# Kernel optimization log

Hardware: AMD Instinct MI355X
Metric: run time of the kernel (lower is better)

The kernel has to match this reference:

```python
import jax, jax.numpy as jnp
import numpy as np

B, H, N, D, RPE = 2, 8, 4096, 64, 64
LAYERS = 3


def _rms(x):
    # SimpleRMSNorm: x / sqrt(mean(x^2) + eps), no learned scale
    return x / jnp.sqrt(jnp.mean(x * x, axis=-1, keepdims=True) + 1e-8)


def setup_inputs() -> dict:
    key = jax.random.key(0)
    ks = jax.random.split(key, 7)
    s = 1.0 / np.sqrt(RPE)
    return {
        "x": jax.random.normal(ks[0], (B, H, N, D), dtype=jnp.float32),
        "w_in": jax.random.normal(ks[1], (1, RPE), dtype=jnp.float32) * 0.5,
        "b_in": jax.random.normal(ks[2], (RPE,), dtype=jnp.float32) * 0.02,
        "w_hid": jax.random.normal(ks[3], (LAYERS, RPE, RPE), dtype=jnp.float32) * s,
        "b_hid": jax.random.normal(ks[4], (LAYERS, RPE), dtype=jnp.float32) * 0.02,
        "w_out": jax.random.normal(ks[5], (RPE, H * D), dtype=jnp.float32) * s,
        "b_out": jax.random.normal(ks[6], (H * D,), dtype=jnp.float32) * 0.02,
    }


def reference(x, w_in, b_in, w_hid, b_hid, w_out, b_out):
    n = x.shape[-2]
    dt = x.dtype

    def rpe(idx):  # idx: (m, 1) relative-position features
        h = idx @ w_in + b_in  # (m, RPE)
        for i in range(LAYERS):  # non-residual: x = layer(x)
            h = jax.nn.relu(_rms(h)) @ w_hid[i] + b_hid[i]
        h = jax.nn.relu(_rms(h)) @ w_out + b_out  # (m, H*D)
        return h.reshape(-1, H, D).transpose(1, 0, 2)  # (H, m, D)

    zero_idx = jnp.ones((1, 1), dt)
    pos_idx = (1.0 / jnp.arange(2, n + 1, dtype=dt)).reshape(n - 1, 1)
    neg_idx = (-1.0 / jnp.arange(n, 1, -1, dtype=dt)).reshape(n - 1, 1)

    zero_k = rpe(zero_idx)  # (H, 1, D); used for both T[0] slots like the torch code
    a = jnp.concatenate([zero_k, rpe(pos_idx), zero_k, rpe(neg_idx)], axis=1)  # (H, 2n, D)
    # act_type='none' -> identity activation on a

    # Toeplitz matvec as circular conv of length 2n via FFT
    y = jnp.fft.rfft(x, 2 * n, axis=-2)          # (B, H, n+1, D) complex
    v = jnp.fft.rfft(a, 2 * n, axis=-2)[None]    # (1, H, n+1, D) complex
    out = jnp.fft.irfft(v * y, 2 * n, axis=-2)[:, :, :n, :]
    return out.astype(dt)
```

## Files before the change

### kernel.cpp

```cpp
#include <hip/hip_runtime.h>

#define N_SEQ 4096
#define N_FFT 8192
#define LAYERS 3
#define FT 512
#define PIDX(i) ((i) + ((i) >> 5))

template<int M>
__device__ inline void pass16_fwd(float* re, float* im, int tid)
{
    const int Q = M >> 4;
    const int j = tid & (Q - 1);
    const int G = tid / Q;
    const int base = G * M + j;
    float xr[4][4], xi[4][4];
#pragma unroll
    for (int a = 0; a < 4; ++a)
#pragma unroll
        for (int b = 0; b < 4; ++b) {
            int idx = PIDX(base + a * (M >> 2) + b * Q);
            xr[a][b] = re[idx]; xi[a][b] = im[idx];
        }
    const float w1 = -6.283185307179586f / (float)M;
#pragma unroll
    for (int b = 0; b < 4; ++b) {
        float ar = xr[0][b] + xr[2][b], ai = xi[0][b] + xi[2][b];
        float br = xr[0][b] - xr[2][b], bi = xi[0][b] - xi[2][b];
        float cr = xr[1][b] + xr[3][b], ci = xi[1][b] + xi[3][b];
        float dr = xi[1][b] - xi[3][b], di = -(xr[1][b] - xr[3][b]);
        float c1, s1; __sincosf(w1 * (float)(b * Q + j), &s1, &c1);
        float c2 = c1 * c1 - s1 * s1, s2 = 2.f * c1 * s1;
        float c3 = c2 * c1 - s2 * s1, s3 = c2 * s1 + s2 * c1;
        xr[0][b] = ar + cr;               xi[0][b] = ai + ci;
        float t1r = br + dr, t1i = bi + di;
        xr[1][b] = t1r * c1 - t1i * s1;   xi[1][b] = t1r * s1 + t1i * c1;
        float t2r = ar - cr, t2i = ai - ci;
        xr[2][b] = t2r * c2 - t2i * s2;   xi[2][b] = t2r * s2 + t2i * c2;
        float t3r = br - dr, t3i = bi - di;
        xr[3][b] = t3r * c3 - t3i * s3;   xi[3][b] = t3r * s3 + t3i * c3;
    }
    {
        const float w4 = -6.283185307179586f / (float)(M >> 2);
        float c1, s1; __sincosf(w4 * (float)j, &s1, &c1);
        float c2 = c1 * c1 - s1 * s1, s2 = 2.f * c1 * s1;
        float c3 = c2 * c1 - s2 * s1, s3 = c2 * s1 + s2 * c1;
#pragma unroll
        for (int a = 0; a < 4; ++a) {
            float ar = xr[a][0] + xr[a][2], ai = xi[a][0] + xi[a][2];
            float br = xr[a][0] - xr[a][2], bi = xi[a][0] - xi[a][2];
            float cr = xr[a][1] + xr[a][3], ci = xi[a][1] + xi[a][3];
            float dr = xi[a][1] - xi[a][3], di = -(xr[a][1] - xr[a][3]);
            xr[a][0] = ar + cr;               xi[a][0] = ai + ci;
            float t1r = br + dr, t1i = bi + di;
            xr[a][1] = t1r * c1 - t1i * s1;   xi[a][1] = t1r * s1 + t1i * c1;
            float t2r = ar - cr, t2i = ai - ci;
            xr[a][2] = t2r * c2 - t2i * s2;   xi[a][2] = t2r * s2 + t2i * c2;
            float t3r = br - dr, t3i = bi - di;
            xr[a][3] = t3r * c3 - t3i * s3;   xi[a][3] = t3r * s3 + t3i * c3;
        }
    }
#pragma unroll
    for (int a = 0; a < 4; ++a)
#pragma unroll
        for (int b = 0; b < 4; ++b) {
            int idx = PIDX(base + a * (M >> 2) + b * Q);
            re[idx] = xr[a][b]; im[idx] = xi[a][b];
        }
}

template<int M>
__device__ inline void pass16_inv(float* re, float* im, int tid)
{
    const int Q = M >> 4;
    const int j = tid & (Q - 1);
    const int G = tid / Q;
    const int base = G * M + j;
    float xr[4][4], xi[4][4];
#pragma unroll
    for (int a = 0; a < 4; ++a)
#pragma unroll
        for (int b = 0; b < 4; ++b) {
            int idx = PIDX(base + a * (M >> 2) + b * Q);
            xr[a][b] = re[idx]; xi[a][b] = im[idx];
        }
    {
        const float w4 = 6.283185307179586f / (float)(M >> 2);
        float c1, s1; __sincosf(w4 * (float)j, &s1, &c1);
        float c2 = c1 * c1 - s1 * s1, s2 = 2.f * c1 * s1;
        float c3 = c2 * c1 - s2 * s1, s3 = c2 * s1 + s2 * c1;
#pragma unroll
        for (int a = 0; a < 4; ++a) {
            float t0r = xr[a][0], t0i = xi[a][0];
            float t1r = xr[a][1] * c1 - xi[a][1] * s1, t1i = xr[a][1] * s1 + xi[a][1] * c1;
            float t2r = xr[a][2] * c2 - xi[a][2] * s2, t2i = xr[a][2] * s2 + xi[a][2] * c2;
            float t3r = xr[a][3] * c3 - xi[a][3] * s3, t3i = xr[a][3] * s3 + xi[a][3] * c3;
            float pr = t0r + t2r, pi = t0i + t2i;
            float qr = t0r - t2r, qi = t0i - t2i;
            float rr = t1r + t3r, ri = t1i + t3i;
            float sr = -(t1i - t3i), si = t1r - t3r;
            xr[a][0] = pr + rr; xi[a][0] = pi + ri;
            xr[a][1] = qr + sr; xi[a][1] = qi + si;
            xr[a][2] = pr - rr; xi[a][2] = pi - ri;
            xr[a][3] = qr - sr; xi[a][3] = qi - si;
        }
    }
    const float w1 = 6.283185307179586f / (float)M;
#pragma unroll
    for (int b = 0; b < 4; ++b) {
        float c1, s1; __sincosf(w1 * (float)(b * Q + j), &s1, &c1);
        float c2 = c1 * c1 - s1 * s1, s2 = 2.f * c1 * s1;
        float c3 = c2 * c1 - s2 * s1, s3 = c2 * s1 + s2 * c1;
        float t0r = xr[0][b], t0i = xi[0][b];
        float t1r = xr[1][b] * c1 - xi[1][b] * s1, t1i = xr[1][b] * s1 + xi[1][b] * c1;
        float t2r = xr[2][b] * c2 - xi[2][b] * s2, t2i = xr[2][b] * s2 + xi[2][b] * c2;
        float t3r = xr[3][b] * c3 - xi[3][b] * s3, t3i = xr[3][b] * s3 + xi[3][b] * c3;
        float pr = t0r + t2r, pi = t0i + t2i;
        float qr = t0r - t2r, qi = t0i - t2i;
        float rr = t1r + t3r, ri = t1i + t3i;
        float sr = -(t1i - t3i), si = t1r - t3r;
        xr[0][b] = pr + rr; xi[0][b] = pi + ri;
        xr[1][b] = qr + sr; xi[1][b] = qi + si;
        xr[2][b] = pr - rr; xi[2][b] = pi - ri;
        xr[3][b] = qr - sr; xi[3][b] = qi - si;
    }
#pragma unroll
    for (int a = 0; a < 4; ++a)
#pragma unroll
        for (int b = 0; b < 4; ++b) {
            int idx = PIDX(base + a * (M >> 2) + b * Q);
            re[idx] = xr[a][b]; im[idx] = xi[a][b];
        }
}

__device__ inline void fwd8(float* zr, float* zi, int o)
{
    const float R = 0.70710678118654752f;
    {
        float ar = zr[o] + zr[o+4], ai = zi[o] + zi[o+4];
        float br = zr[o] - zr[o+4], bi = zi[o] - zi[o+4];
        float cr = zr[o+2] + zr[o+6], ci = zi[o+2] + zi[o+6];
        float dr = zi[o+2] - zi[o+6], di = -(zr[o+2] - zr[o+6]);
        zr[o]   = ar + cr; zi[o]   = ai + ci;
        zr[o+2] = br + dr; zi[o+2] = bi + di;
        zr[o+4] = ar - cr; zi[o+4] = ai - ci;
        zr[o+6] = br - dr; zi[o+6] = bi - di;
    }
    {
        float ar = zr[o+1] + zr[o+5], ai = zi[o+1] + zi[o+5];
        float br = zr[o+1] - zr[o+5], bi = zi[o+1] - zi[o+5];
        float cr = zr[o+3] + zr[o+7], ci = zi[o+3] + zi[o+7];
        float dr = zi[o+3] - zi[o+7], di = -(zr[o+3] - zr[o+7]);
        zr[o+1] = ar + cr; zi[o+1] = ai + ci;
        float t1r = br + dr, t1i = bi + di;
        zr[o+3] = R * (t1r + t1i); zi[o+3] = R * (t1i - t1r);
        float t2r = ar - cr, t2i = ai - ci;
        zr[o+5] = t2i;  zi[o+5] = -t2r;
        float t3r = br - dr, t3i = bi - di;
        zr[o+7] = R * (t3i - t3r); zi[o+7] = -R * (t3r + t3i);
    }
#pragma unroll
    for (int p = 0; p < 8; p += 2) {
        float ur = zr[o+p], ui = zi[o+p], vr = zr[o+p+1], vi = zi[o+p+1];
        zr[o+p]   = ur + vr; zi[o+p]   = ui + vi;
        zr[o+p+1] = ur - vr; zi[o+p+1] = ui - vi;
    }
}

__device__ inline void inv8(float* zr, float* zi, int o)
{
    const float R = 0.70710678118654752f;
#pragma unroll
    for (int p = 0; p < 8; p += 2) {
        float ur = zr[o+p], ui = zi[o+p], vr = zr[o+p+1], vi = zi[o+p+1];
        zr[o+p]   = ur + vr; zi[o+p]   = ui + vi;
        zr[o+p+1] = ur - vr; zi[o+p+1] = ui - vi;
    }
    {
        float t0r = zr[o],   t0i = zi[o];
        float t1r = zr[o+2], t1i = zi[o+2];
        float t2r = zr[o+4], t2i = zi[o+4];
        float t3r = zr[o+6], t3i = zi[o+6];
        float pr = t0r + t2r, pi = t0i + t2i;
        float qr = t0r - t2r, qi = t0i - t2i;
        float rr = t1r + t3r, ri = t1i + t3i;
        float sr = -(t1i - t3i), si = t1r - t3r;
        zr[o]   = pr + rr; zi[o]   = pi + ri;
        zr[o+2] = qr + sr; zi[o+2] = qi + si;
        zr[o+4] = pr - rr; zi[o+4] = pi - ri;
        zr[o+6] = qr - sr; zi[o+6] = qi - si;
    }
    {
        float t0r = zr[o+1], t0i = zi[o+1];
        float yr = zr[o+3], yi = zi[o+3];
        float t1r = R * (yr - yi), t1i = R * (yr + yi);
        yr = zr[o+5]; yi = zi[o+5];
        float t2r = -yi, t2i = yr;
        yr = zr[o+7]; yi = zi[o+7];
        float t3r = -R * (yr + yi), t3i = R * (yr - yi);
        float pr = t0r + t2r, pi = t0i + t2i;
        float qr = t0r - t2r, qi = t0i - t2i;
        float rr = t1r + t3r, ri = t1i + t3i;
        float sr = -(t1i - t3i), si = t1r - t3r;
        zr[o+1] = pr + rr; zi[o+1] = pi + ri;
        zr[o+3] = qr + sr; zi[o+3] = qi + si;
        zr[o+5] = pr - rr; zi[o+5] = pi - ri;
        zr[o+7] = qr - sr; zi[o+7] = qi - si;
    }
}

__global__ __launch_bounds__(256) void rpe_hidden_kernel(
    const float* __restrict__ w_in, const float* __restrict__ b_in,
    const float* __restrict__ w_hid, const float* __restrict__ b_hid,
    float* __restrict__ u_t)
{
    __shared__ float4 wl[1024];
    __shared__ float ubuf[64][65];
    __shared__ float sums[64][5];
    const int tid = threadIdx.x;
    const int p   = tid & 63;
    const int qr  = tid >> 6;
    const int pos = blockIdx.x * 64 + p;

    float v;
    if (pos == 0 || pos == N_SEQ) v = 1.0f;
    else if (pos < N_SEQ)         v = 1.0f / (float)(pos + 1);
    else                          v = -1.0f / (float)(2 * N_SEQ + 1 - pos);

    float h[16];
#pragma unroll
    for (int i = 0; i < 16; ++i) {
        int f = qr * 16 + i;
        h[i] = v * w_in[f] + b_in[f];
    }
    for (int L = 0; L < LAYERS; ++L) {
        const float4* wsrc = (const float4*)(w_hid + L * 4096);
#pragma unroll
        for (int i = 0; i < 4; ++i) wl[i * 256 + tid] = wsrc[i * 256 + tid];
        float s = 0.f;
#pragma unroll
        for (int i = 0; i < 16; ++i) s += h[i] * h[i];
        sums[p][qr] = s;
        __syncthreads();
        float tot = sums[p][0] + sums[p][1] + sums[p][2] + sums[p][3];
        float r = rsqrtf(tot * (1.f / 64.f) + 1e-8f);
#pragma unroll
        for (int i = 0; i < 16; ++i)
            ubuf[p][qr * 16 + i] = fmaxf(h[i] * r, 0.f);
        __syncthreads();
        float acc[16];
#pragma unroll
        for (int i = 0; i < 16; ++i) acc[i] = b_hid[L * 64 + qr * 16 + i];
#pragma unroll 4
        for (int j = 0; j < 64; ++j) {
            float uj = ubuf[p][j];
            float4 w0 = wl[j * 16 + qr * 4 + 0];
            float4 w1 = wl[j * 16 + qr * 4 + 1];
            float4 w2 = wl[j * 16 + qr * 4 + 2];
            float4 w3 = wl[j * 16 + qr * 4 + 3];
            acc[0]  = fmaf(uj, w0.x, acc[0]);  acc[1]  = fmaf(uj, w0.y, acc[1]);
            acc[2]  = fmaf(uj, w0.z, acc[2]);  acc[3]  = fmaf(uj, w0.w, acc[3]);
            acc[4]  = fmaf(uj, w1.x, acc[4]);  acc[5]  = fmaf(uj, w1.y, acc[5]);
            acc[6]  = fmaf(uj, w1.z, acc[6]);  acc[7]  = fmaf(uj, w1.w, acc[7]);
            acc[8]  = fmaf(uj, w2.x, acc[8]);  acc[9]  = fmaf(uj, w2.y, acc[9]);
            acc[10] = fmaf(uj, w2.z, acc[10]); acc[11] = fmaf(uj, w2.w, acc[11]);
            acc[12] = fmaf(uj, w3.x, acc[12]); acc[13] = fmaf(uj, w3.y, acc[13]);
            acc[14] = fmaf(uj, w3.z, acc[14]); acc[15] = fmaf(uj, w3.w, acc[15]);
        }
#pragma unroll
        for (int i = 0; i < 16; ++i) h[i] = acc[i];
        __syncthreads();
    }
    float s = 0.f;
#pragma unroll
    for (int i = 0; i < 16; ++i) s += h[i] * h[i];
    sums[p][qr] = s;
    __syncthreads();
    float tot = sums[p][0] + sums[p][1] + sums[p][2] + sums[p][3];
    float r = rsqrtf(tot * (1.f / 64.f) + 1e-8f);
#pragma unroll
    for (int i = 0; i < 16; ++i)
        u_t[(size_t)(qr * 16 + i) * N_FFT + pos] = fmaxf(h[i] * r, 0.f);
}

__global__ __launch_bounds__(256) void rpe_out_kernel(
    const float* __restrict__ u_t, const float* __restrict__ w_out,
    const float* __restrict__ b_out, float* __restrict__ a_t)
{
    __shared__ float4 wl[1024];
    const int tid = threadIdx.x;
    const int c   = blockIdx.y;
    const int pos = blockIdx.x * 256 + tid;
    for (int i = tid; i < 1024; i += 256) {
        int j = i >> 4, q = i & 15;
        wl[i] = *(const float4*)(w_out + j * 512 + c * 64 + q * 4);
    }
    float acc[64];
#pragma unroll
    for (int f = 0; f < 64; ++f) acc[f] = b_out[c * 64 + f];
    __syncthreads();
#pragma unroll 2
    for (int j = 0; j < 64; ++j) {
        float uj = u_t[(size_t)j * N_FFT + pos];
#pragma unroll
        for (int q = 0; q < 16; ++q) {
            float4 w4 = wl[j * 16 + q];
            acc[q * 4 + 0] = fmaf(uj, w4.x, acc[q * 4 + 0]);
            acc[q * 4 + 1] = fmaf(uj, w4.y, acc[q * 4 + 1]);
            acc[q * 4 + 2] = fmaf(uj, w4.z, acc[q * 4 + 2]);
            acc[q * 4 + 3] = fmaf(uj, w4.w, acc[q * 4 + 3]);
        }
    }
#pragma unroll
    for (int f = 0; f < 64; ++f)
        a_t[(size_t)(c * 64 + f) * N_FFT + pos] = acc[f];
}

__global__ __launch_bounds__(FT, 4) void fft_a_kernel(const float* __restrict__ a_t,
                                                      float2* __restrict__ Af)
{
    __shared__ float re[8448];
    __shared__ float im[8448];
    const int tid = threadIdx.x;
    const size_t row = blockIdx.x;
    const float* src = a_t + row * N_FFT;
    const float wstep = -6.283185307179586f / 8192.f;
#pragma unroll
    for (int k = tid; k < 2048; k += FT) {
        float x0 = src[k], x1 = src[k + 2048], x2 = src[k + 4096], x3 = src[k + 6144];
        float ar = x0 + x2, br = x0 - x2;
        float cr = x1 + x3, e = x1 - x3;
        re[PIDX(k)] = ar + cr; im[PIDX(k)] = 0.f;
        float c1, s1; __sincosf(wstep * (float)k, &s1, &c1);
        float c2 = c1 * c1 - s1 * s1, s2 = 2.f * c1 * s1;
        float c3 = c2 * c1 - s2 * s1, s3 = c2 * s1 + s2 * c1;
        re[PIDX(k + 2048)] = br * c1 + e * s1;  im[PIDX(k + 2048)] = br * s1 - e * c1;
        float t2r = ar - cr;
        re[PIDX(k + 4096)] = t2r * c2;          im[PIDX(k + 4096)] = t2r * s2;
        re[PIDX(k + 6144)] = br * c3 - e * s3;  im[PIDX(k + 6144)] = br * s3 + e * c3;
    }
    __syncthreads();
    pass16_fwd<2048>(re, im, tid);
    __syncthreads();
    pass16_fwd<128>(re, im, tid);
    __syncthreads();
    float zr[16], zi[16];
    const int base = tid * 16;
#pragma unroll
    for (int c = 0; c < 16; ++c) { int idx = PIDX(base + c); zr[c] = re[idx]; zi[c] = im[idx]; }
    fwd8(zr, zi, 0); fwd8(zr, zi, 8);
    const float inv = 1.0f / (float)N_FFT;
    float4* dst4 = (float4*)(Af + row * N_FFT + base);
#pragma unroll
    for (int q = 0; q < 8; ++q)
        dst4[q] = make_float4(zr[2*q] * inv, zi[2*q] * inv, zr[2*q+1] * inv, zi[2*q+1] * inv);
}

__global__ __launch_bounds__(256) void transpose_x_kernel(const float* __restrict__ x,
                                                          float2* __restrict__ xt2)
{
    __shared__ float t0[64][65];
    __shared__ float t1[64][65];
    int h = blockIdx.x >> 6;
    int nb = blockIdx.x & 63;
    int lx = threadIdx.x & 63;
    int ly = threadIdx.x >> 6;
    const float* s0 = x + ((size_t)h * N_SEQ + nb * 64) * 64;
    const float* s1 = x + ((size_t)(8 + h) * N_SEQ + nb * 64) * 64;
    for (int r = ly; r < 64; r += 4) {
        t0[r][lx] = s0[r * 64 + lx];
        t1[r][lx] = s1[r * 64 + lx];
    }
    __syncthreads();
    for (int r = ly; r < 64; r += 4) {
        float2* dst = xt2 + (size_t)(h * 64 + r) * N_SEQ + nb * 64;
        dst[lx] = make_float2(t0[lx][r], t1[lx][r]);
    }
}

__global__ __launch_bounds__(FT, 4) void conv_kernel(const float2* __restrict__ xt2,
                                                     const float2* __restrict__ Af,
                                                     float2* __restrict__ out_t2)
{
    __shared__ float re[8448];
    __shared__ float im[8448];
    const int tid = threadIdx.x;
    const int hd = blockIdx.x;
    const float2* src = xt2 + (size_t)hd * N_SEQ;
    {
        const float wstep = -6.283185307179586f / 8192.f;
#pragma unroll
        for (int k = tid; k < 2048; k += FT) {
            float2 z0 = src[k], z1 = src[k + 2048];
            float ar = z0.x, ai = z0.y;
            float cr = z1.x, ci = z1.y;
            float dr = z1.y, di = -z1.x;
            re[PIDX(k)] = ar + cr; im[PIDX(k)] = ai + ci;
            float c1, s1; __sincosf(wstep * (float)k, &s1, &c1);
            float c2 = c1 * c1 - s1 * s1, s2 = 2.f * c1 * s1;
            float c3 = c2 * c1 - s2 * s1, s3 = c2 * s1 + s2 * c1;
            float t1r = ar + dr, t1i = ai + di;
            re[PIDX(k + 2048)] = t1r * c1 - t1i * s1; im[PIDX(k + 2048)] = t1r * s1 + t1i * c1;
            float t2r = ar - cr, t2i = ai - ci;
            re[PIDX(k + 4096)] = t2r * c2 - t2i * s2; im[PIDX(k + 4096)] = t2r * s2 + t2i * c2;
            float t3r = ar - dr, t3i = ai - di;
            re[PIDX(k + 6144)] = t3r * c3 - t3i * s3; im[PIDX(k + 6144)] = t3r * s3 + t3i * c3;
        }
    }
    __syncthreads();
    pass16_fwd<2048>(re, im, tid);
    __syncthreads();
    pass16_fwd<128>(re, im, tid);
    __syncthreads();
    {
        float zr[16], zi[16];
        const int base = tid * 16;
#pragma unroll
        for (int c = 0; c < 16; ++c) { int idx = PIDX(base + c); zr[c] = re[idx]; zi[c] = im[idx]; }
        fwd8(zr, zi, 0); fwd8(zr, zi, 8);
        const float4* af4 = (const float4*)(Af + (size_t)hd * N_FFT + base);
#pragma unroll
        for (int q = 0; q < 8; ++q) {
            float4 a4 = af4[q];
            float xr = zr[2*q], xi_ = zi[2*q];
            zr[2*q]   = xr * a4.x - xi_ * a4.y;  zi[2*q]   = xr * a4.y + xi_ * a4.x;
            xr = zr[2*q+1]; xi_ = zi[2*q+1];
            zr[2*q+1] = xr * a4.z - xi_ * a4.w;  zi[2*q+1] = xr * a4.w + xi_ * a4.z;
        }
        inv8(zr, zi, 0); inv8(zr, zi, 8);
#pragma unroll
        for (int c = 0; c < 16; ++c) { int idx = PIDX(base + c); re[idx] = zr[c]; im[idx] = zi[c]; }
    }
    __syncthreads();
    pass16_inv<128>(re, im, tid);
    __syncthreads();
    pass16_inv<2048>(re, im, tid);
    __syncthreads();
    {
        const float wstep = 6.283185307179586f / 8192.f;
        float2* dst = out_t2 + (size_t)hd * N_SEQ;
#pragma unroll
        for (int k = tid; k < 2048; k += FT) {
            float c1, s1; __sincosf(wstep * (float)k, &s1, &c1);
            float c2 = c1 * c1 - s1 * s1, s2 = 2.f * c1 * s1;
            float c3 = c2 * c1 - s2 * s1, s3 = c2 * s1 + s2 * c1;
            float t0r = re[PIDX(k)],        t0i = im[PIDX(k)];
            float y1r = re[PIDX(k + 2048)], y1i = im[PIDX(k + 2048)];
            float y2r = re[PIDX(k + 4096)], y2i = im[PIDX(k + 4096)];
            float y3r = re[PIDX(k + 6144)], y3i = im[PIDX(k + 6144)];
            float t1r = y1r * c1 - y1i * s1, t1i = y1r * s1 + y1i * c1;
            float t2r = y2r * c2 - y2i * s2, t2i = y2r * s2 + y2i * c2;
            float t3r = y3r * c3 - y3i * s3, t3i = y3r * s3 + y3i * c3;
            float pr = t0r + t2r, pi = t0i + t2i;
            float qr = t0r - t2r, qi = t0i - t2i;
            float rr = t1r + t3r, ri = t1i + t3i;
            float sr = -(t1i - t3i), si = t1r - t3r;
            dst[k]        = make_float2(pr + rr, pi + ri);
            dst[k + 2048] = make_float2(qr + sr, qi + si);
        }
    }
}

__global__ __launch_bounds__(256) void transpose_o_kernel(const float2* __restrict__ out_t2,
                                                          float* __restrict__ out)
{
    __shared__ float t0[64][65];
    __shared__ float t1[64][65];
    int h = blockIdx.x >> 6;
    int nb = blockIdx.x & 63;
    int lx = threadIdx.x & 63;
    int ly = threadIdx.x >> 6;
    for (int r = ly; r < 64; r += 4) {
        float2 v = out_t2[(size_t)(h * 64 + r) * N_SEQ + nb * 64 + lx];
        t0[r][lx] = v.x;
        t1[r][lx] = v.y;
    }
    __syncthreads();
    float* d0 = out + ((size_t)h * N_SEQ + nb * 64) * 64;
    float* d1 = out + ((size_t)(8 + h) * N_SEQ + nb * 64) * 64;
    for (int r = ly; r < 64; r += 4) {
        d0[r * 64 + lx] = t0[lx][r];
        d1[r * 64 + lx] = t1[lx][r];
    }
}

extern "C" void kernel_launch(void* const* d_in, const int* in_sizes, int n_in,
                              void* d_out, int out_size, void* d_ws, size_t ws_size,
                              hipStream_t stream)
{
    const float* x     = (const float*)d_in[0];
    const float* w_in  = (const float*)d_in[1];
    const float* b_in  = (const float*)d_in[2];
    const float* w_hid = (const float*)d_in[3];
    const float* b_hid = (const float*)d_in[4];
    const float* w_out = (const float*)d_in[5];
    const float* b_out = (const float*)d_in[6];
    float* out = (float*)d_out;

    char* ws = (char*)d_ws;
    float2* Af    = (float2*)ws;
    float2* xt2   = (float2*)(ws + (size_t)32 * 1024 * 1024);
    float*  a_t   = (float*)(ws + (size_t)48 * 1024 * 1024);
    float*  u_t   = (float*)xt2;
    float2* out_t2 = (float2*)a_t;

    rpe_hidden_kernel<<<128, 256, 0, stream>>>(w_in, b_in, w_hid, b_hid, u_t);
    rpe_out_kernel<<<dim3(32, 8), 256, 0, stream>>>(u_t, w_out, b_out, a_t);
    fft_a_kernel<<<512, FT, 0, stream>>>(a_t, Af);
    transpose_x_kernel<<<512, 256, 0, stream>>>(x, xt2);
    conv_kernel<<<512, FT, 0, stream>>>(xt2, Af, out_t2);
    transpose_o_kernel<<<512, 256, 0, stream>>>(out_t2, out);
}
```

Baseline: 174.3 us.

## Fuse RPE MLP, x transpose, and kernel FFT into fewer launches

Merges the RPE hidden layers and output projection into one prep kernel that also runs the x transpose on extra blocks. The kernel FFT moves into the conv kernel, where the filter spectrum is kept in registers instead of being written to and read back from global memory. Per-element __sincosf calls in the FFT passes are replaced by one sincos per thread plus constant rotations and recurrences. This cuts launches and global traffic, but raises register pressure in conv_kernel, repeats the filter FFT inside every conv block, and may slightly reduce twiddle accuracy.

```diff
diff --git a/kernel.cpp b/kernel.cpp
--- a/kernel.cpp
+++ b/kernel.cpp
@@ -13,6 +13,8 @@
     const int j = tid & (Q - 1);
     const int G = tid / Q;
     const int base = G * M + j;
+    const float KR[4] = {1.f, 0.9238795325f, 0.7071067812f, 0.3826834324f};
+    const float KI[4] = {0.f, -0.3826834324f, -0.7071067812f, -0.9238795325f};
     float xr[4][4], xi[4][4];
 #pragma unroll
     for (int a = 0; a < 4; ++a)
@@ -21,16 +23,18 @@
             int idx = PIDX(base + a * (M >> 2) + b * Q);
             xr[a][b] = re[idx]; xi[a][b] = im[idx];
         }
-    const float w1 = -6.283185307179586f / (float)M;
+    float cj, sj;
+    __sincosf(-6.283185307179586f / (float)M * (float)j, &sj, &cj);
 #pragma unroll
     for (int b = 0; b < 4; ++b) {
+        float c1 = cj * KR[b] - sj * KI[b];
+        float s1 = cj * KI[b] + sj * KR[b];
+        float c2 = c1 * c1 - s1 * s1, s2 = 2.f * c1 * s1;
+        float c3 = c2 * c1 - s2 * s1, s3 = c2 * s1 + s2 * c1;
         float ar = xr[0][b] + xr[2][b], ai = xi[0][b] + xi[2][b];
         float br = xr[0][b] - xr[2][b], bi = xi[0][b] - xi[2][b];
         float cr = xr[1][b] + xr[3][b], ci = xi[1][b] + xi[3][b];
         float dr = xi[1][b] - xi[3][b], di = -(xr[1][b] - xr[3][b]);
-        float c1, s1; __sincosf(w1 * (float)(b * Q + j), &s1, &c1);
-        float c2 = c1 * c1 - s1 * s1, s2 = 2.f * c1 * s1;
-        float c3 = c2 * c1 - s2 * s1, s3 = c2 * s1 + s2 * c1;
         xr[0][b] = ar + cr;               xi[0][b] = ai + ci;
         float t1r = br + dr, t1i = bi + di;
         xr[1][b] = t1r * c1 - t1i * s1;   xi[1][b] = t1r * s1 + t1i * c1;
@@ -40,8 +44,8 @@
         xr[3][b] = t3r * c3 - t3i * s3;   xi[3][b] = t3r * s3 + t3i * c3;
     }
     {
-        const float w4 = -6.283185307179586f / (float)(M >> 2);
-        float c1, s1; __sincosf(w4 * (float)j, &s1, &c1);
+        float e1c = cj * cj - sj * sj, e1s = 2.f * cj * sj;
+        float c1 = e1c * e1c - e1s * e1s, s1 = 2.f * e1c * e1s;
         float c2 = c1 * c1 - s1 * s1, s2 = 2.f * c1 * s1;
         float c3 = c2 * c1 - s2 * s1, s3 = c2 * s1 + s2 * c1;
 #pragma unroll
@@ -75,6 +79,8 @@
     const int j = tid & (Q - 1);
     const int G = tid / Q;
     const int base = G * M + j;
+    const float KR[4] = {1.f, 0.9238795325f, 0.7071067812f, 0.3826834324f};
+    const float KI[4] = {0.f, 0.3826834324f, 0.7071067812f, 0.9238795325f};
     float xr[4][4], xi[4][4];
 #pragma unroll
     for (int a = 0; a < 4; ++a)
@@ -83,9 +89,11 @@
             int idx = PIDX(base + a * (M >> 2) + b * Q);
             xr[a][b] = re[idx]; xi[a][b] = im[idx];
         }
-    {
-        const float w4 = 6.283185307179586f / (float)(M >> 2);
-        float c1, s1; __sincosf(w4 * (float)j, &s1, &c1);
+    float cj, sj;
+    __sincosf(6.283185307179586f / (float)M * (float)j, &sj, &cj);
+    {
+        float e1c = cj * cj - sj * sj, e1s = 2.f * cj * sj;
+        float c1 = e1c * e1c - e1s * e1s, s1 = 2.f * e1c * e1s;
         float c2 = c1 * c1 - s1 * s1, s2 = 2.f * c1 * s1;
         float c3 = c2 * c1 - s2 * s1, s3 = c2 * s1 + s2 * c1;
 #pragma unroll
@@ -104,10 +112,10 @@
             xr[a][3] = qr - sr; xi[a][3] = qi - si;
         }
     }
-    const float w1 = 6.283185307179586f / (float)M;
 #pragma unroll
     for (int b = 0; b < 4; ++b) {
-        float c1, s1; __sincosf(w1 * (float)(b * Q + j), &s1, &c1);
+        float c1 = cj * KR[b] - sj * KI[b];
+        float s1 = cj * KI[b] + sj * KR[b];
         float c2 = c1 * c1 - s1 * s1, s2 = 2.f * c1 * s1;
         float c3 = c2 * c1 - s2 * s1, s3 = c2 * s1 + s2 * c1;
         float t0r = xr[0][b], t0i = xi[0][b];
@@ -208,28 +216,54 @@
     }
 }
 
-__global__ __launch_bounds__(256) void rpe_hidden_kernel(
+__global__ __launch_bounds__(256) void prep_kernel(
+    const float* __restrict__ x,
     const float* __restrict__ w_in, const float* __restrict__ b_in,
     const float* __restrict__ w_hid, const float* __restrict__ b_hid,
-    float* __restrict__ u_t)
-{
-    __shared__ float4 wl[1024];
-    __shared__ float ubuf[64][65];
-    __shared__ float sums[64][5];
+    const float* __restrict__ w_out, const float* __restrict__ b_out,
+    float* __restrict__ a_t, float2* __restrict__ xt2)
+{
+    __shared__ __align__(16) char smem[33536];
     const int tid = threadIdx.x;
-    const int p   = tid & 63;
-    const int qr  = tid >> 6;
-    const int pos = blockIdx.x * 64 + p;
+
+    if (blockIdx.x >= 256) {
+        float (*t0)[65] = (float (*)[65])smem;
+        float (*t1)[65] = (float (*)[65])(smem + 16640);
+        int bb = blockIdx.x - 256;
+        int h = bb >> 6;
+        int nb = bb & 63;
+        int lx = tid & 63;
+        int ly = tid >> 6;
+        const float* s0 = x + ((size_t)h * N_SEQ + nb * 64) * 64;
+        const float* s1 = x + ((size_t)(8 + h) * N_SEQ + nb * 64) * 64;
+        for (int r = ly; r < 64; r += 4) {
+            t0[r][lx] = s0[r * 64 + lx];
+            t1[r][lx] = s1[r * 64 + lx];
+        }
+        __syncthreads();
+        for (int r = ly; r < 64; r += 4) {
+            float2* dst = xt2 + (size_t)(h * 64 + r) * N_SEQ + nb * 64;
+            dst[lx] = make_float2(t0[lx][r], t1[lx][r]);
+        }
+        return;
+    }
+
+    float4* wl       = (float4*)smem;
+    float (*ubuf)[65] = (float (*)[65])(smem + 16384);
+    float (*sums)[9]  = (float (*)[9])(smem + 24704);
+    const int p   = tid & 31;
+    const int oct = tid >> 5;
+    const int pos = blockIdx.x * 32 + p;
 
     float v;
     if (pos == 0 || pos == N_SEQ) v = 1.0f;
     else if (pos < N_SEQ)         v = 1.0f / (float)(pos + 1);
     else                          v = -1.0f / (float)(2 * N_SEQ + 1 - pos);
 
-    float h[16];
-#pragma unroll
-    for (int i = 0; i < 16; ++i) {
-        int f = qr * 16 + i;
+    float h[8];
+#pragma unroll
+    for (int i = 0; i < 8; ++i) {
+        int f = oct * 8 + i;
         h[i] = v * w_in[f] + b_in[f];
     }
     for (int L = 0; L < LAYERS; ++L) {
@@ -238,164 +272,142 @@
         for (int i = 0; i < 4; ++i) wl[i * 256 + tid] = wsrc[i * 256 + tid];
         float s = 0.f;
 #pragma unroll
-        for (int i = 0; i < 16; ++i) s += h[i] * h[i];
-        sums[p][qr] = s;
-        __syncthreads();
-        float tot = sums[p][0] + sums[p][1] + sums[p][2] + sums[p][3];
+        for (int i = 0; i < 8; ++i) s += h[i] * h[i];
+        sums[p][oct] = s;
+        __syncthreads();
+        float tot = 0.f;
+#pragma unroll
+        for (int g = 0; g < 8; ++g) tot += sums[p][g];
         float r = rsqrtf(tot * (1.f / 64.f) + 1e-8f);
 #pragma unroll
-        for (int i = 0; i < 16; ++i)
-            ubuf[p][qr * 16 + i] = fmaxf(h[i] * r, 0.f);
-        __syncthreads();
-        float acc[16];
-#pragma unroll
-        for (int i = 0; i < 16; ++i) acc[i] = b_hid[L * 64 + qr * 16 + i];
+        for (int i = 0; i < 8; ++i)
+            ubuf[p][oct * 8 + i] = fmaxf(h[i] * r, 0.f);
+        __syncthreads();
+        float acc[8];
+#pragma unroll
+        for (int i = 0; i < 8; ++i) acc[i] = b_hid[L * 64 + oct * 8 + i];
 #pragma unroll 4
         for (int j = 0; j < 64; ++j) {
             float uj = ubuf[p][j];
-            float4 w0 = wl[j * 16 + qr * 4 + 0];
-            float4 w1 = wl[j * 16 + qr * 4 + 1];
-            float4 w2 = wl[j * 16 + qr * 4 + 2];
-            float4 w3 = wl[j * 16 + qr * 4 + 3];
-            acc[0]  = fmaf(uj, w0.x, acc[0]);  acc[1]  = fmaf(uj, w0.y, acc[1]);
-            acc[2]  = fmaf(uj, w0.z, acc[2]);  acc[3]  = fmaf(uj, w0.w, acc[3]);
-            acc[4]  = fmaf(uj, w1.x, acc[4]);  acc[5]  = fmaf(uj, w1.y, acc[5]);
-            acc[6]  = fmaf(uj, w1.z, acc[6]);  acc[7]  = fmaf(uj, w1.w, acc[7]);
-            acc[8]  = fmaf(uj, w2.x, acc[8]);  acc[9]  = fmaf(uj, w2.y, acc[9]);
-            acc[10] = fmaf(uj, w2.z, acc[10]); acc[11] = fmaf(uj, w2.w, acc[11]);
-            acc[12] = fmaf(uj, w3.x, acc[12]); acc[13] = fmaf(uj, w3.y, acc[13]);
-            acc[14] = fmaf(uj, w3.z, acc[14]); acc[15] = fmaf(uj, w3.w, acc[15]);
-        }
-#pragma unroll
-        for (int i = 0; i < 16; ++i) h[i] = acc[i];
-        __syncthreads();
-    }
-    float s = 0.f;
-#pragma unroll
-    for (int i = 0; i < 16; ++i) s += h[i] * h[i];
-    sums[p][qr] = s;
-    __syncthreads();
-    float tot = sums[p][0] + sums[p][1] + sums[p][2] + sums[p][3];
-    float r = rsqrtf(tot * (1.f / 64.f) + 1e-8f);
-#pragma unroll
-    for (int i = 0; i < 16; ++i)
-        u_t[(size_t)(qr * 16 + i) * N_FFT + pos] = fmaxf(h[i] * r, 0.f);
-}
-
-__global__ __launch_bounds__(256) void rpe_out_kernel(
-    const float* __restrict__ u_t, const float* __restrict__ w_out,
-    const float* __restrict__ b_out, float* __restrict__ a_t)
-{
-    __shared__ float4 wl[1024];
-    const int tid = threadIdx.x;
-    const int c   = blockIdx.y;
-    const int pos = blockIdx.x * 256 + tid;
-    for (int i = tid; i < 1024; i += 256) {
-        int j = i >> 4, q = i & 15;
-        wl[i] = *(const float4*)(w_out + j * 512 + c * 64 + q * 4);
-    }
-    float acc[64];
-#pragma unroll
-    for (int f = 0; f < 64; ++f) acc[f] = b_out[c * 64 + f];
-    __syncthreads();
-#pragma unroll 2
-    for (int j = 0; j < 64; ++j) {
-        float uj = u_t[(size_t)j * N_FFT + pos];
-#pragma unroll
-        for (int q = 0; q < 16; ++q) {
-            float4 w4 = wl[j * 16 + q];
-            acc[q * 4 + 0] = fmaf(uj, w4.x, acc[q * 4 + 0]);
-            acc[q * 4 + 1] = fmaf(uj, w4.y, acc[q * 4 + 1]);
-            acc[q * 4 + 2] = fmaf(uj, w4.z, acc[q * 4 + 2]);
-            acc[q * 4 + 3] = fmaf(uj, w4.w, acc[q * 4 + 3]);
-        }
-    }
-#pragma unroll
-    for (int f = 0; f < 64; ++f)
-        a_t[(size_t)(c * 64 + f) * N_FFT + pos] = acc[f];
-}
-
-__global__ __launch_bounds__(FT, 4) void fft_a_kernel(const float* __restrict__ a_t,
-                                                      float2* __restrict__ Af)
-{
-    __shared__ float re[8448];
-    __shared__ float im[8448];
-    const int tid = threadIdx.x;
-    const size_t row = blockIdx.x;
-    const float* src = a_t + row * N_FFT;
-    const float wstep = -6.283185307179586f / 8192.f;
-#pragma unroll
-    for (int k = tid; k < 2048; k += FT) {
-        float x0 = src[k], x1 = src[k + 2048], x2 = src[k + 4096], x3 = src[k + 6144];
-        float ar = x0 + x2, br = x0 - x2;
-        float cr = x1 + x3, e = x1 - x3;
-        re[PIDX(k)] = ar + cr; im[PIDX(k)] = 0.f;
-        float c1, s1; __sincosf(wstep * (float)k, &s1, &c1);
-        float c2 = c1 * c1 - s1 * s1, s2 = 2.f * c1 * s1;
-        float c3 = c2 * c1 - s2 * s1, s3 = c2 * s1 + s2 * c1;
-        re[PIDX(k + 2048)] = br * c1 + e * s1;  im[PIDX(k + 2048)] = br * s1 - e * c1;
-        float t2r = ar - cr;
-        re[PIDX(k + 4096)] = t2r * c2;          im[PIDX(k + 4096)] = t2r * s2;
-        re[PIDX(k + 6144)] = br * c3 - e * s3;  im[PIDX(k + 6144)] = br * s3 + e * c3;
-    }
-    __syncthreads();
-    pass16_fwd<2048>(re, im, tid);
-    __syncthreads();
-    pass16_fwd<128>(re, im, tid);
-    __syncthreads();
-    float zr[16], zi[16];
-    const int base = tid * 16;
-#pragma unroll
-    for (int c = 0; c < 16; ++c) { int idx = PIDX(base + c); zr[c] = re[idx]; zi[c] = im[idx]; }
-    fwd8(zr, zi, 0); fwd8(zr, zi, 8);
-    const float inv = 1.0f / (float)N_FFT;
-    float4* dst4 = (float4*)(Af + row * N_FFT + base);
-#pragma unroll
-    for (int q = 0; q < 8; ++q)
-        dst4[q] = make_float4(zr[2*q] * inv, zi[2*q] * inv, zr[2*q+1] * inv, zi[2*q+1] * inv);
-}
-
-__global__ __launch_bounds__(256) void transpose_x_kernel(const float* __restrict__ x,
-                                                          float2* __restrict__ xt2)
-{
-    __shared__ float t0[64][65];
-    __shared__ float t1[64][65];
-    int h = blockIdx.x >> 6;
-    int nb = blockIdx.x & 63;
-    int lx = threadIdx.x & 63;
-    int ly = threadIdx.x >> 6;
-    const float* s0 = x + ((size_t)h * N_SEQ + nb * 64) * 64;
-    const float* s1 = x + ((size_t)(8 + h) * N_SEQ + nb * 64) * 64;
-    for (int r = ly; r < 64; r += 4) {
-        t0[r][lx] = s0[r * 64 + lx];
-        t1[r][lx] = s1[r * 64 + lx];
-    }
-    __syncthreads();
-    for (int r = ly; r < 64; r += 4) {
-        float2* dst = xt2 + (size_t)(h * 64 + r) * N_SEQ + nb * 64;
-        dst[lx] = make_float2(t0[lx][r], t1[lx][r]);
-    }
-}
-
-__global__ __launch_bounds__(FT, 4) void conv_kernel(const float2* __restrict__ xt2,
-                                                     const float2* __restrict__ Af,
+            float4 w0 = wl[j * 16 + oct * 2];
+            float4 w1 = wl[j * 16 + oct * 2 + 1];
+            acc[0] = fmaf(uj, w0.x, acc[0]); acc[1] = fmaf(uj, w0.y, acc[1]);
+            acc[2] = fmaf(uj, w0.z, acc[2]); acc[3] = fmaf(uj, w0.w, acc[3]);
+            acc[4] = fmaf(uj, w1.x, acc[4]); acc[5] = fmaf(uj, w1.y, acc[5]);
+            acc[6] = fmaf(uj, w1.z, acc[6]); acc[7] = fmaf(uj, w1.w, acc[7]);
+        }
+#pragma unroll
+        for (int i = 0; i < 8; ++i) h[i] = acc[i];
+        __syncthreads();
+    }
+    {
+        float s = 0.f;
+#pragma unroll
+        for (int i = 0; i < 8; ++i) s += h[i] * h[i];
+        sums[p][oct] = s;
+        __syncthreads();
+        float tot = 0.f;
+#pragma unroll
+        for (int g = 0; g < 8; ++g) tot += sums[p][g];
+        float r = rsqrtf(tot * (1.f / 64.f) + 1e-8f);
+#pragma unroll
+        for (int i = 0; i < 8; ++i)
+            ubuf[p][oct * 8 + i] = fmaxf(h[i] * r, 0.f);
+        __syncthreads();
+    }
+    for (int c = 0; c < 8; ++c) {
+        float4 wreg[4];
+#pragma unroll
+        for (int cc = 0; cc < 4; ++cc) {
+            int i4 = cc * 256 + tid;
+            int j = i4 >> 4, q = i4 & 15;
+            wreg[cc] = *(const float4*)(w_out + j * 512 + c * 64 + q * 4);
+        }
+        __syncthreads();
+#pragma unroll
+        for (int cc = 0; cc < 4; ++cc) wl[cc * 256 + tid] = wreg[cc];
+        __syncthreads();
+        float acc[8];
+#pragma unroll
+        for (int i = 0; i < 8; ++i) acc[i] = b_out[c * 64 + oct * 8 + i];
+#pragma unroll 4
+        for (int j = 0; j < 64; ++j) {
+            float uj = ubuf[p][j];
+            float4 w0 = wl[j * 16 + oct * 2];
+            float4 w1 = wl[j * 16 + oct * 2 + 1];
+            acc[0] = fmaf(uj, w0.x, acc[0]); acc[1] = fmaf(uj, w0.y, acc[1]);
+            acc[2] = fmaf(uj, w0.z, acc[2]); acc[3] = fmaf(uj, w0.w, acc[3]);
+            acc[4] = fmaf(uj, w1.x, acc[4]); acc[5] = fmaf(uj, w1.y, acc[5]);
+            acc[6] = fmaf(uj, w1.z, acc[6]); acc[7] = fmaf(uj, w1.w, acc[7]);
+        }
+#pragma unroll
+        for (int i = 0; i < 8; ++i)
+            a_t[(size_t)(c * 64 + oct * 8 + i) * N_FFT + pos] = acc[i];
+    }
+}
+
+__global__ __launch_bounds__(FT, 4) void conv_kernel(const float* __restrict__ a_t,
+                                                     const float2* __restrict__ xt2,
                                                      float2* __restrict__ out_t2)
 {
     __shared__ float re[8448];
     __shared__ float im[8448];
     const int tid = threadIdx.x;
     const int hd = blockIdx.x;
-    const float2* src = xt2 + (size_t)hd * N_SEQ;
-    {
-        const float wstep = -6.283185307179586f / 8192.f;
-#pragma unroll
-        for (int k = tid; k < 2048; k += FT) {
+    const float JR = 0.9238795325f;
+    const float JI = -0.3826834324f;
+
+    {
+        const float* src = a_t + (size_t)hd * N_FFT;
+        float ck, sk;
+        __sincosf(-6.283185307179586f / 8192.f * (float)tid, &sk, &ck);
+#pragma unroll
+        for (int pp = 0; pp < 4; ++pp) {
+            int k = pp * FT + tid;
+            float x0 = src[k], x1 = src[k + 2048], x2 = src[k + 4096], x3 = src[k + 6144];
+            float ar = x0 + x2, br = x0 - x2;
+            float cr = x1 + x3, e = x1 - x3;
+            re[PIDX(k)] = ar + cr; im[PIDX(k)] = 0.f;
+            float c1 = ck, s1 = sk;
+            float c2 = c1 * c1 - s1 * s1, s2 = 2.f * c1 * s1;
+            float c3 = c2 * c1 - s2 * s1, s3 = c2 * s1 + s2 * c1;
+            re[PIDX(k + 2048)] = br * c1 + e * s1;  im[PIDX(k + 2048)] = br * s1 - e * c1;
+            float t2r = ar - cr;
+            re[PIDX(k + 4096)] = t2r * c2;          im[PIDX(k + 4096)] = t2r * s2;
+            re[PIDX(k + 6144)] = br * c3 - e * s3;  im[PIDX(k + 6144)] = br * s3 + e * c3;
+            float tc = ck * JR - sk * JI; sk = ck * JI + sk * JR; ck = tc;
+        }
+    }
+    __syncthreads();
+    pass16_fwd<2048>(re, im, tid);
+    __syncthreads();
+    pass16_fwd<128>(re, im, tid);
+    __syncthreads();
+    float afr[16], afi[16];
+    {
+        const int base = tid * 16;
+        float zr[16], zi[16];
+#pragma unroll
+        for (int c = 0; c < 16; ++c) { int idx = PIDX(base + c); zr[c] = re[idx]; zi[c] = im[idx]; }
+        fwd8(zr, zi, 0); fwd8(zr, zi, 8);
+        const float inv = 1.0f / (float)N_FFT;
+#pragma unroll
+        for (int c = 0; c < 16; ++c) { afr[c] = zr[c] * inv; afi[c] = zi[c] * inv; }
+    }
+    __syncthreads();
+    {
+        const float2* src = xt2 + (size_t)hd * N_SEQ;
+        float ck, sk;
+        __sincosf(-6.283185307179586f / 8192.f * (float)tid, &sk, &ck);
+#pragma unroll
+        for (int pp = 0; pp < 4; ++pp) {
+            int k = pp * FT + tid;
             float2 z0 = src[k], z1 = src[k + 2048];
             float ar = z0.x, ai = z0.y;
             float cr = z1.x, ci = z1.y;
             float dr = z1.y, di = -z1.x;
             re[PIDX(k)] = ar + cr; im[PIDX(k)] = ai + ci;
-            float c1, s1; __sincosf(wstep * (float)k, &s1, &c1);
+            float c1 = ck, s1 = sk;
             float c2 = c1 * c1 - s1 * s1, s2 = 2.f * c1 * s1;
             float c3 = c2 * c1 - s2 * s1, s3 = c2 * s1 + s2 * c1;
             float t1r = ar + dr, t1i = ai + di;
@@ -404,6 +416,7 @@
             re[PIDX(k + 4096)] = t2r * c2 - t2i * s2; im[PIDX(k + 4096)] = t2r * s2 + t2i * c2;
             float t3r = ar - dr, t3i = ai - di;
             re[PIDX(k + 6144)] = t3r * c3 - t3i * s3; im[PIDX(k + 6144)] = t3r * s3 + t3i * c3;
+            float tc = ck * JR - sk * JI; sk = ck * JI + sk * JR; ck = tc;
         }
     }
     __syncthreads();
@@ -412,19 +425,16 @@
     pass16_fwd<128>(re, im, tid);
     __syncthreads();
     {
+        const int base = tid * 16;
         float zr[16], zi[16];
-        const int base = tid * 16;
 #pragma unroll
         for (int c = 0; c < 16; ++c) { int idx = PIDX(base + c); zr[c] = re[idx]; zi[c] = im[idx]; }
         fwd8(zr, zi, 0); fwd8(zr, zi, 8);
-        const float4* af4 = (const float4*)(Af + (size_t)hd * N_FFT + base);
-#pragma unroll
-        for (int q = 0; q < 8; ++q) {
-            float4 a4 = af4[q];
-            float xr = zr[2*q], xi_ = zi[2*q];
-            zr[2*q]   = xr * a4.x - xi_ * a4.y;  zi[2*q]   = xr * a4.y + xi_ * a4.x;
-            xr = zr[2*q+1]; xi_ = zi[2*q+1];
-            zr[2*q+1] = xr * a4.z - xi_ * a4.w;  zi[2*q+1] = xr * a4.w + xi_ * a4.z;
+#pragma unroll
+        for (int c = 0; c < 16; ++c) {
+            float xr = zr[c], xi_ = zi[c];
+            zr[c] = xr * afr[c] - xi_ * afi[c];
+            zi[c] = xr * afi[c] + xi_ * afr[c];
         }
         inv8(zr, zi, 0); inv8(zr, zi, 8);
 #pragma unroll
@@ -436,11 +446,14 @@
     pass16_inv<2048>(re, im, tid);
     __syncthreads();
     {
-        const float wstep = 6.283185307179586f / 8192.f;
         float2* dst = out_t2 + (size_t)hd * N_SEQ;
-#pragma unroll
-        for (int k = tid; k < 2048; k += FT) {
-            float c1, s1; __sincosf(wstep * (float)k, &s1, &c1);
+        float ck, sk;
+        __sincosf(6.283185307179586f / 8192.f * (float)tid, &sk, &ck);
+        const float JcR = 0.9238795325f, JcI = 0.3826834324f;
+#pragma unroll
+        for (int pp = 0; pp < 4; ++pp) {
+            int k = pp * FT + tid;
+            float c1 = ck, s1 = sk;
             float c2 = c1 * c1 - s1 * s1, s2 = 2.f * c1 * s1;
             float c3 = c2 * c1 - s2 * s1, s3 = c2 * s1 + s2 * c1;
             float t0r = re[PIDX(k)],        t0i = im[PIDX(k)];
@@ -456,6 +469,7 @@
             float sr = -(t1i - t3i), si = t1r - t3r;
             dst[k]        = make_float2(pr + rr, pi + ri);
             dst[k + 2048] = make_float2(qr + sr, qi + si);
+            float tc = ck * JcR - sk * JcI; sk = ck * JcI + sk * JcR; ck = tc;
         }
     }
 }
@@ -497,16 +511,12 @@
     float* out = (float*)d_out;
 
     char* ws = (char*)d_ws;
-    float2* Af    = (float2*)ws;
-    float2* xt2   = (float2*)(ws + (size_t)32 * 1024 * 1024);
-    float*  a_t   = (float*)(ws + (size_t)48 * 1024 * 1024);
-    float*  u_t   = (float*)xt2;
-    float2* out_t2 = (float2*)a_t;
-
-    rpe_hidden_kernel<<<128, 256, 0, stream>>>(w_in, b_in, w_hid, b_hid, u_t);
-    rpe_out_kernel<<<dim3(32, 8), 256, 0, stream>>>(u_t, w_out, b_out, a_t);
-    fft_a_kernel<<<512, FT, 0, stream>>>(a_t, Af);
-    transpose_x_kernel<<<512, 256, 0, stream>>>(x, xt2);
-    conv_kernel<<<512, FT, 0, stream>>>(xt2, Af, out_t2);
+    float2* xt2    = (float2*)ws;
+    float*  a_t    = (float*)(ws + (size_t)16 * 1024 * 1024);
+    float2* out_t2 = (float2*)(ws + (size_t)32 * 1024 * 1024);
+
+    prep_kernel<<<768, 256, 0, stream>>>(x, w_in, b_in, w_hid, b_hid, w_out, b_out,
+                                         a_t, xt2);
+    conv_kernel<<<512, FT, 0, stream>>>(a_t, xt2, out_t2);
     transpose_o_kernel<<<512, 256, 0, stream>>>(out_t2, out);
 }
```

Measured after the change: 169.7 us. -2.6%, faster.
